# Kernel tuning notes

Hardware: AMD Instinct MI355X
Metric: run time of the kernel (lower is better)

## Reference

```python
import jax, jax.numpy as jnp
import numpy as np

NPOINT = 2048  # S after transition-down (init npoint)
NSAMPLE = 16   # K neighbors (init nsample)
EPS = 1e-5     # BatchNorm eps


def _conv1d(w, b, x):  # w [O,I], x [B,I,N] -> [B,O,N]
    y = jnp.einsum('oi,bin->bon', w, x)
    return y if b is None else y + b[None, :, None]


def _conv2d(w, b, x):  # w [O,I], x [B,I,S,K] -> [B,O,S,K]
    y = jnp.einsum('oi,bisk->bosk', w, x)
    return y if b is None else y + b[None, :, None, None]


def _gather(x, idx):  # x [B,C,N], idx [B,S] -> [B,C,S]
    return jax.vmap(lambda xb, ib: xb[:, ib])(x, idx)


def _group(x, idx):  # x [B,C,N], idx [B,S,K] -> [B,C,S,K]
    return jax.vmap(lambda xb, ib: xb[:, ib])(x, idx)


def _fps(xyz_bnc, S):  # farthest point sampling, start at index 0 (deterministic)
    B, N, _ = xyz_bnc.shape
    def body(carry, _):
        dist, far = carry
        centroid = jnp.take_along_axis(xyz_bnc, far[:, None, None], axis=1)  # [B,1,3]
        d = jnp.sum((xyz_bnc - centroid) ** 2, axis=-1)  # [B,N]
        dist = jnp.minimum(dist, d)
        nxt = jnp.argmax(dist, axis=-1).astype(jnp.int32)
        return (dist, nxt), far
    init = (jnp.full((B, N), 1e10, xyz_bnc.dtype), jnp.zeros((B,), jnp.int32))
    _, idxs = jax.lax.scan(body, init, None, length=S)
    return jnp.transpose(idxs)  # [B,S]


def _knn(k, query, pts):  # query [B,S,3], pts [B,N,3] -> idx [B,S,k]
    d2 = (jnp.sum(query ** 2, -1)[..., None] + jnp.sum(pts ** 2, -1)[:, None, :]
          - 2.0 * jnp.einsum('bsc,bnc->bsn', query, pts))
    _, idx = jax.lax.top_k(-d2, k)
    return idx


def _bn(x, gamma, beta):  # training-mode batchnorm over (B, spatial) per channel
    axes = (0,) + tuple(range(2, x.ndim))
    m = jnp.mean(x, axes, keepdims=True)
    v = jnp.var(x, axes, keepdims=True)
    shp = (1, -1) + (1,) * (x.ndim - 2)
    return gamma.reshape(shp) * (x - m) / jnp.sqrt(v + EPS) + beta.reshape(shp)


def _forward(xyz, points, td_w, td_b, td_gamma, td_beta,
             blk_before_w, blk_before_b, blk_qkv_w,
             blk_pos_w1, blk_pos_b1, blk_pos_w2, blk_pos_b2,
             blk_attn_w1, blk_attn_b1, blk_attn_w2, blk_attn_b2,
             blk_after_w, blk_after_b):
    S, K = NPOINT, NSAMPLE
    xyz_t = jnp.transpose(xyz, (0, 2, 1))  # [B,N,3]
    # ---- PointTransformerTransitionDown ----
    fps_idx = _fps(xyz_t, S)                       # [B,S]
    new_xyz = _gather(xyz, fps_idx)                # [B,3,S]
    new_xyz_t = jnp.transpose(new_xyz, (0, 2, 1))  # [B,S,3]
    gidx = _knn(K, new_xyz_t, xyz_t)               # [B,S,K]
    grouped_xyz = _group(xyz, gidx) - new_xyz[:, :, :, None]   # [B,3,S,K]
    grouped = jnp.concatenate([_group(points, gidx), grouped_xyz], axis=1)  # [B,D+3,S,K]
    h = jax.nn.relu(_bn(_conv2d(td_w, td_b, grouped), td_gamma, td_beta))
    pts = jnp.max(h, axis=-1)  # [B,out,S]
    # ---- PointTransformerResBlocks ----
    sgidx = _knn(K, new_xyz_t, new_xyz_t)          # self-KNN [B,S,K]
    gxyz = new_xyz[:, :, :, None] - _group(new_xyz, sgidx)  # [B,3,S,K]
    num_attn = blk_before_w.shape[0]
    for i in range(num_attn):
        rel = _conv2d(blk_pos_w2[i], blk_pos_b2[i],
                      jax.nn.relu(_conv2d(blk_pos_w1[i], blk_pos_b1[i], gxyz)))  # [B,mid,S,K]
        p = _conv1d(blk_before_w[i], blk_before_b[i], pts)   # [B,mid,S]
        qkv = _conv1d(blk_qkv_w[i], None, p)                 # [B,3*mid,S]
        q, k_, v = jnp.split(qkv, 3, axis=1)
        qk_rel = q[:, :, :, None] - _group(k_, sgidx)        # [B,mid,S,K]
        v = _group(v, sgidx) + rel
        sim = _conv2d(blk_attn_w2[i], blk_attn_b2[i],
                      jax.nn.relu(_conv2d(blk_attn_w1[i], blk_attn_b1[i], qk_rel + rel)))
        attn = jax.nn.softmax(sim, axis=-1)                  # softmax over neighbors
        agg = jnp.sum(attn * v, axis=-1)                     # [B,mid,S]
        pts = pts + _conv1d(blk_after_w[i], blk_after_b[i], agg)
    return new_xyz, pts


def setup_inputs() -> dict:
    key = jax.random.key(0)
    ks = jax.random.split(key, 20)
    B, N, Din, Dout, mid, A = 4, 8192, 64, 128, 32, 2
    r = lambda k, s, sc: sc * jax.random.normal(k, s, dtype=jnp.float32)
    return {
        'xyz': r(ks[0], (B, 3, N), 1.0),
        'points': r(ks[1], (B, Din, N), 1.0),
        'td_w': r(ks[2], (Dout, Din + 3), 0.1), 'td_b': r(ks[3], (Dout,), 0.02),
        'td_gamma': jnp.ones((Dout,), jnp.float32), 'td_beta': jnp.zeros((Dout,), jnp.float32),
        'blk_before_w': r(ks[4], (A, mid, Dout), 0.1), 'blk_before_b': r(ks[5], (A, mid), 0.02),
        'blk_qkv_w': r(ks[6], (A, 3 * mid, mid), 0.1),
        'blk_pos_w1': r(ks[7], (A, 64, 3), 0.1), 'blk_pos_b1': r(ks[8], (A, 64), 0.02),
        'blk_pos_w2': r(ks[9], (A, mid, 64), 0.1), 'blk_pos_b2': r(ks[10], (A, mid), 0.02),
        'blk_attn_w1': r(ks[11], (A, 4 * mid, mid), 0.1), 'blk_attn_b1': r(ks[12], (A, 4 * mid), 0.02),
        'blk_attn_w2': r(ks[13], (A, mid, 4 * mid), 0.1), 'blk_attn_b2': r(ks[14], (A, mid), 0.02),
        'blk_after_w': r(ks[15], (A, Dout, mid), 0.1), 'blk_after_b': r(ks[16], (A, Dout), 0.02),
    }


def reference(xyz, points, td_w, td_b, td_gamma, td_beta,
              blk_before_w, blk_before_b, blk_qkv_w,
              blk_pos_w1, blk_pos_b1, blk_pos_w2, blk_pos_b2,
              blk_attn_w1, blk_attn_b1, blk_attn_w2, blk_attn_b2,
              blk_after_w, blk_after_b):
    return _forward(xyz, points, td_w, td_b, td_gamma, td_beta,
                    blk_before_w, blk_before_b, blk_qkv_w,
                    blk_pos_w1, blk_pos_b1, blk_pos_w2, blk_pos_b2,
                    blk_attn_w1, blk_attn_b1, blk_attn_w2, blk_attn_b2,
                    blk_after_w, blk_after_b)
```

## Files before the change

kernel.cpp:

```cpp
#include <hip/hip_runtime.h>

#define BB 4
#define NN 8192
#define SS 2048
#define KK 16

typedef float v2f __attribute__((ext_vector_type(2)));

#define FTH 512
#define FPT (NN/FTH)
#define TRB 256
#define SPB 124
__global__ __launch_bounds__(FTH, 1) void fps_kernel(
    const float* __restrict__ xyz,
    const float* __restrict__ points,
    float* __restrict__ out_newxyz,
    float* __restrict__ nxt,
    float* __restrict__ ptst,
    int* __restrict__ spin_flag)
{
  #pragma clang fp contract(off)
  const int blk = blockIdx.x;
  const int tid = threadIdx.x;
  __shared__ __align__(16) float4 sxyz[NN];
  __shared__ __align__(16) unsigned long long skey[2][8];
  __shared__ int smi[SS];
  __shared__ float sred[8*6];
  __shared__ float tile[32][33];

  if (blk >= BB) {
    if (blk < BB + TRB) {
      const int x = tid & 31, yy = tid >> 5;
      for (int q = 0; q < 8; ++q) {
        const int tj = (blk - BB)*8 + q;
        const int tn = tj & 255, tc = (tj >> 8) & 1, tb = tj >> 9;
        const int n0 = tn*32, c0 = tc*32;
        __syncthreads();
        tile[yy][x]    = points[(tb*64 + c0+yy)*NN + n0+x];
        tile[yy+16][x] = points[(tb*64 + c0+yy+16)*NN + n0+x];
        __syncthreads();
        ptst[(tb*NN + n0+yy)*64 + c0+x]    = tile[x][yy];
        ptst[(tb*NN + n0+yy+16)*64 + c0+x] = tile[x][yy+16];
      }
      return;
    }
    if (tid >= 64) return;
    const int s0 = atomicAdd(spin_flag, 0);
    float a0 = 1.0f + tid, a1 = 2.0f, a2 = 3.0f, a3 = 4.0f;
    for (int outer = 0; outer < 50000; ++outer) {
      #pragma unroll
      for (int u = 0; u < 256; ++u) {
        a0 = fmaf(a0, 1.0000001f, 1e-7f);
        a1 = fmaf(a1, 0.9999999f, 2e-7f);
        a2 = fmaf(a2, 1.0000002f, 3e-7f);
        a3 = fmaf(a3, 0.9999998f, 4e-7f);
      }
      if (atomicAdd(spin_flag, 0) - s0 >= BB) break;
    }
    asm volatile("" :: "v"(a0), "v"(a1), "v"(a2), "v"(a3));
    return;
  }

  const int b = blk;
  const int wave = tid >> 6;
  const int lane = tid & 63;
  const float* xb = xyz + b*3*NN;

  float tx[FPT], ty[FPT], tz[FPT];
  #pragma unroll
  for (int j = 0; j < FPT; ++j) {
    int i = tid + j*FTH;
    tx[j] = xb[i]; ty[j] = xb[NN+i]; tz[j] = xb[2*NN+i];
  }
  float mnx = tx[0], mxx = tx[0], mny = ty[0], mxy = ty[0], mnz = tz[0], mxz = tz[0];
  #pragma unroll
  for (int j = 1; j < FPT; ++j) {
    mnx = fminf(mnx, tx[j]); mxx = fmaxf(mxx, tx[j]);
    mny = fminf(mny, ty[j]); mxy = fmaxf(mxy, ty[j]);
    mnz = fminf(mnz, tz[j]); mxz = fmaxf(mxz, tz[j]);
  }
  #define WRED(var, OP) { \
    float s_; \
    s_ = __int_as_float(__builtin_amdgcn_update_dpp(0, __float_as_int(var), 0x111, 0xf, 0xf, true)); var = OP(var, s_); \
    s_ = __int_as_float(__builtin_amdgcn_update_dpp(0, __float_as_int(var), 0x112, 0xf, 0xf, true)); var = OP(var, s_); \
    s_ = __int_as_float(__builtin_amdgcn_update_dpp(0, __float_as_int(var), 0x114, 0xf, 0xf, true)); var = OP(var, s_); \
    s_ = __int_as_float(__builtin_amdgcn_update_dpp(0, __float_as_int(var), 0x118, 0xf, 0xf, true)); var = OP(var, s_); \
    s_ = __int_as_float(__builtin_amdgcn_update_dpp(0, __float_as_int(var), 0x142, 0xf, 0xf, true)); var = OP(var, s_); \
    s_ = __int_as_float(__builtin_amdgcn_update_dpp(0, __float_as_int(var), 0x143, 0xf, 0xf, true)); var = OP(var, s_); }
  WRED(mnx, fminf) WRED(mxx, fmaxf) WRED(mny, fminf) WRED(mxy, fmaxf) WRED(mnz, fminf) WRED(mxz, fmaxf)
  #undef WRED
  if (lane == 63) {
    sred[wave*6+0] = mnx; sred[wave*6+1] = mxx; sred[wave*6+2] = mny;
    sred[wave*6+3] = mxy; sred[wave*6+4] = mnz; sred[wave*6+5] = mxz;
  }
  smi[tid] = 0;
  __syncthreads();
  #pragma unroll
  for (int w = 0; w < 8; ++w) {
    mnx = fminf(mnx, sred[w*6+0]); mxx = fmaxf(mxx, sred[w*6+1]);
    mny = fminf(mny, sred[w*6+2]); mxy = fmaxf(mxy, sred[w*6+3]);
    mnz = fminf(mnz, sred[w*6+4]); mxz = fmaxf(mxz, sred[w*6+5]);
  }
  const float scx = 8.0f / (mxx - mnx + 1e-12f);
  const float scy = 8.0f / (mxy - mny + 1e-12f);
  const float scz = 8.0f / (mxz - mnz + 1e-12f);
  int cells[FPT];
  #pragma unroll
  for (int j = 0; j < FPT; ++j) {
    int qx = min(7, (int)((tx[j] - mnx) * scx));
    int qy = min(7, (int)((ty[j] - mny) * scy));
    int qz = min(7, (int)((tz[j] - mnz) * scz));
    int m = (qx&1) | ((qy&1)<<1) | ((qz&1)<<2)
          | ((qx&2)<<2) | ((qy&2)<<3) | ((qz&2)<<4)
          | ((qx&4)<<4) | ((qy&4)<<5) | ((qz&4)<<6);
    cells[j] = m;
    atomicAdd(&smi[m], 1);
  }
  __syncthreads();
  for (int d = 1; d < 512; d <<= 1) {
    int v = smi[tid];
    int a = (tid >= d) ? smi[tid - d] : 0;
    __syncthreads();
    smi[tid] = v + a;
    __syncthreads();
  }
  {
    int excl = (tid == 0) ? 0 : smi[tid - 1];
    smi[512 + tid] = excl;
  }
  __syncthreads();
  #pragma unroll
  for (int j = 0; j < FPT; ++j) {
    int pos = atomicAdd(&smi[512 + cells[j]], 1);
    sxyz[pos] = make_float4(tx[j], ty[j], tz[j], 0.0f);
  }
  __syncthreads();
  v2f px[FPT/2], py[FPT/2], pz[FPT/2], dist[FPT/2];
  float bx0, bx1, by0, by1, bz0, bz1;
  {
    float4 c0 = sxyz[tid*FPT];
    bx0 = bx1 = c0.x; by0 = by1 = c0.y; bz0 = bz1 = c0.z;
    #pragma unroll
    for (int e = 0; e < FPT; ++e) {
      float4 cc = sxyz[tid*FPT + e];
      ((float*)px)[e] = cc.x; ((float*)py)[e] = cc.y; ((float*)pz)[e] = cc.z;
      ((float*)dist)[e] = 1e10f;
      bx0 = fminf(bx0, cc.x); bx1 = fmaxf(bx1, cc.x);
      by0 = fminf(by0, cc.y); by1 = fmaxf(by1, cc.y);
      bz0 = fminf(bz0, cc.z); bz1 = fmaxf(bz1, cc.z);
    }
  }
  float dmax = 1e10f;
  int   beste = 0;
  float cx = xb[0], cy = xb[NN], cz = xb[2*NN];
  __syncthreads();
  for (int it = 1; it < SS; ++it) {
    const int buf = it & 1;
    float gx = fmaxf(fmaxf(bx0 - cx, cx - bx1), 0.0f);
    float gy = fmaxf(fmaxf(by0 - cy, cy - by1), 0.0f);
    float gz = fmaxf(fmaxf(bz0 - cz, cz - bz1), 0.0f);
    float lb = gx*gx + gy*gy; lb = lb + gz*gz;
    if (lb * 0.99999f < dmax) {
      v2f cx2 = {cx, cx}, cy2 = {cy, cy}, cz2 = {cz, cz};
      v2f vmax = {-1.0f, -1.0f};
      #pragma unroll
      for (int j = 0; j < FPT/2; ++j) {
        v2f dx = px[j] - cx2, dy = py[j] - cy2, dz = pz[j] - cz2;
        v2f d = dx*dx + dy*dy;
        d = d + dz*dz;
        v2f nd = __builtin_elementwise_min(dist[j], d);
        dist[j] = nd;
        vmax = __builtin_elementwise_max(vmax, nd);
      }
      float mloc = fmaxf(vmax.x, vmax.y);
      int ce[FPT/2];
      #pragma unroll
      for (int j = 0; j < FPT/2; ++j) {
        int c = 0x7FFFFFFF;
        if (dist[j].y == mloc) c = 2*j + 1;
        if (dist[j].x == mloc) c = 2*j;
        ce[j] = c;
      }
      #pragma unroll
      for (int st = FPT/4; st >= 1; st >>= 1) {
        #pragma unroll
        for (int j = 0; j < st; ++j) ce[j] = ce[j] < ce[j+st] ? ce[j] : ce[j+st];
      }
      dmax = mloc;
      beste = ce[0];
    }
    unsigned khi = __float_as_uint(dmax);
    unsigned klo = ~(unsigned)((tid << 4) + beste);
    #define FPS_RED(ctrl) { \
      unsigned nlo = (unsigned)__builtin_amdgcn_update_dpp(0, (int)klo, ctrl, 0xf, 0xf, true); \
      unsigned nhi = (unsigned)__builtin_amdgcn_update_dpp(0, (int)khi, ctrl, 0xf, 0xf, true); \
      unsigned long long nk = ((unsigned long long)nhi << 32) | nlo; \
      unsigned long long ck = ((unsigned long long)khi << 32) | klo; \
      if (nk > ck) { khi = nhi; klo = nlo; } }
    FPS_RED(0x111)
    FPS_RED(0x112)
    FPS_RED(0x114)
    FPS_RED(0x118)
    FPS_RED(0x142)
    FPS_RED(0x143)
    #undef FPS_RED
    if (lane == 63) skey[buf][wave] = ((unsigned long long)khi << 32) | klo;
    __syncthreads();
    const ulonglong2* kp = (const ulonglong2*)&skey[buf][0];
    ulonglong2 k01 = kp[0], k23 = kp[1], k45 = kp[2], k67 = kp[3];
    unsigned long long m0 = k01.x > k01.y ? k01.x : k01.y;
    unsigned long long m1 = k23.x > k23.y ? k23.x : k23.y;
    unsigned long long m2 = k45.x > k45.y ? k45.x : k45.y;
    unsigned long long m3 = k67.x > k67.y ? k67.x : k67.y;
    unsigned long long ma = m0 > m1 ? m0 : m1;
    unsigned long long mb = m2 > m3 ? m2 : m3;
    unsigned long long mk = ma > mb ? ma : mb;
    int mi = (int)(~(unsigned)mk);
    float4 c = sxyz[mi];
    if (tid == 0) smi[it] = mi;
    cx = c.x; cy = c.y; cz = c.z;
  }
  __syncthreads();
  for (int it = tid; it < SS; it += FTH) {
    float x, y, z;
    if (it == 0) { x = xb[0]; y = xb[NN]; z = xb[2*NN]; }
    else { float4 c = sxyz[smi[it]]; x = c.x; y = c.y; z = c.z; }
    out_newxyz[(b*3+0)*SS + it] = x;
    out_newxyz[(b*3+1)*SS + it] = y;
    out_newxyz[(b*3+2)*SS + it] = z;
    nxt[(b*SS+it)*3+0] = x; nxt[(b*SS+it)*3+1] = y; nxt[(b*SS+it)*3+2] = z;
  }
  if (tid == 0) atomicAdd(spin_flag, 1);
}

#define TILE 2048
#define KTH 512
__global__ __launch_bounds__(KTH) void knn_kernel(
    const float* __restrict__ query_t,
    const float* __restrict__ cand1,
    const float* __restrict__ cand2,
    int* __restrict__ out1,
    int* __restrict__ out2)
{
  #pragma clang fp contract(off)
  __shared__ float4 sc[TILE];
  __shared__ float  smd[8*64*17];
  __shared__ int    smj[8*64*17];
  const int blocksPerB = SS/64;
  const int half = blockIdx.x >> 7;
  const int blk = blockIdx.x & 127;
  const float* cand = half ? cand2 : cand1;
  const int Nc = half ? SS : NN;
  int* outidx = half ? out2 : out1;
  const int b = blk / blocksPerB;
  const int q0 = (blk % blocksPerB)*64;
  const int wave = threadIdx.x >> 6, lane = threadIdx.x & 63;
  const int s = q0 + lane;
  const float qx = query_t[(b*SS+s)*3+0];
  const float qy = query_t[(b*SS+s)*3+1];
  const float qz = query_t[(b*SS+s)*3+2];
  float sq = qx*qx + qy*qy; sq = sq + qz*qz;
  float d16[16]; int i16[16];
  #pragma unroll
  for (int j = 0; j < 16; ++j) { d16[j] = 1e30f; i16[j] = 0x7FFFFFFF; }
  const float* cb = cand + b*3*Nc;
  const int QL = TILE/8;
  for (int base = 0; base < Nc; base += TILE) {
    __syncthreads();
    for (int j = threadIdx.x; j < TILE; j += KTH) {
      float x = cb[base+j], y = cb[Nc+base+j], z = cb[2*Nc+base+j];
      float pp = x*x + y*y; pp = pp + z*z;
      sc[j] = make_float4(x, y, z, pp);
    }
    __syncthreads();
    const int lo = wave*QL, hi = lo + QL;
    for (int j = lo; j < hi; ++j) {
      float4 c = sc[j];
      float qp = qx*c.x + qy*c.y; qp = qp + qz*c.z;
      float d2 = (sq + c.w) - 2.0f*qp;
      if (d2 < d16[15]) {
        d16[15] = d2; i16[15] = base + j;
        #pragma unroll
        for (int t = 15; t > 0; --t) {
          if (d16[t] < d16[t-1]) {
            float td = d16[t]; d16[t] = d16[t-1]; d16[t-1] = td;
            int   ti = i16[t]; i16[t] = i16[t-1]; i16[t-1] = ti;
          }
        }
      }
    }
  }
  const int off = (wave*64 + lane)*17;
  #pragma unroll
  for (int j = 0; j < 16; ++j) { smd[off+j] = d16[j]; smj[off+j] = i16[j]; }
  __syncthreads();
  if (wave == 0) {
    int p[8] = {0,0,0,0,0,0,0,0};
    for (int o = 0; o < 16; ++o) {
      float bd = 3e38f; int bi = 0x7FFFFFFF, bw = 0;
      #pragma unroll
      for (int w = 0; w < 8; ++w) {
        float d = smd[(w*64+lane)*17 + p[w]];
        int   i = smj[(w*64+lane)*17 + p[w]];
        if (d < bd || (d == bd && i < bi)) { bd = d; bi = i; bw = w; }
      }
      p[bw]++;
      outidx[(b*SS+s)*KK + o] = bi;
    }
  }
}

__global__ __launch_bounds__(128) void td_kernel(
    const float* __restrict__ ptst,
    const float* __restrict__ xyz,
    const float* __restrict__ newxyz,
    const int* __restrict__ gidx,
    const float* __restrict__ td_w,
    const float* __restrict__ td_b,
    float* __restrict__ ymax,
    float* __restrict__ psum,
    float* __restrict__ psq)
{
  const int bs = blockIdx.x;
  const int b = bs >> 11, s = bs & (SS-1);
  const int t = threadIdx.x;
  __shared__ int gi[KK];
  __shared__ float g[67*17];
  if (t < KK) gi[t] = gidx[bs*KK + t];
  __syncthreads();
  #pragma unroll
  for (int base = 0; base < 1024; base += 128) {
    int idx = base + t;
    int i = idx & 63, k = idx >> 6;
    g[i*17 + k] = ptst[(b*NN + gi[k])*64 + i];
  }
  if (t < 48) {
    int c = t >> 4, k = t & 15;
    g[(64+c)*17 + k] = xyz[(b*3+c)*NN + gi[k]] - newxyz[(b*3+c)*SS + s];
  }
  __syncthreads();
  float acc[KK];
  #pragma unroll
  for (int k = 0; k < KK; ++k) acc[k] = 0.0f;
  const float* wrow = td_w + t*67;
  for (int i = 0; i < 67; ++i) {
    float w = wrow[i];
    #pragma unroll
    for (int k = 0; k < KK; ++k) acc[k] = fmaf(w, g[i*17 + k], acc[k]);
  }
  float bias = td_b[t];
  float mx = -1e30f, s1 = 0.f, s2 = 0.f;
  #pragma unroll
  for (int k = 0; k < KK; ++k) {
    float y = acc[k] + bias;
    mx = fmaxf(mx, y);
    s1 += y;
    s2 = fmaf(y, y, s2);
  }
  ymax[bs*128 + t] = mx;
  psum[bs*128 + t] = s1;
  psq [bs*128 + t] = s2;
}

__global__ __launch_bounds__(256) void bn_partial(
    const float* __restrict__ psum, const float* __restrict__ psq,
    float* __restrict__ part1, float* __restrict__ part2)
{
  const int blk = blockIdx.x, t = threadIdx.x;
  const int c = t & 127, half = t >> 7;
  const float* ps = psum + (blk*64 + half*32)*128;
  const float* pq = psq  + (blk*64 + half*32)*128;
  float s1 = 0.f, s2 = 0.f;
  for (int r = 0; r < 32; ++r) { s1 += ps[r*128 + c]; s2 += pq[r*128 + c]; }
  __shared__ float sh1[256], sh2[256];
  sh1[t] = s1; sh2[t] = s2;
  __syncthreads();
  if (t < 128) {
    part1[blk*128 + t] = sh1[t] + sh1[t+128];
    part2[blk*128 + t] = sh2[t] + sh2[t+128];
  }
}

__global__ __launch_bounds__(128) void bn_final(
    const float* __restrict__ part1, const float* __restrict__ part2,
    const float* __restrict__ gamma, const float* __restrict__ beta,
    float* __restrict__ scale, float* __restrict__ bias)
{
  const int o = threadIdx.x;
  float s1 = 0.f, s2 = 0.f;
  for (int j = 0; j < 128; ++j) { s1 += part1[j*128+o]; s2 += part2[j*128+o]; }
  const float n = (float)(BB*SS*KK);
  float mean = s1/n;
  float var  = s2/n - mean*mean;
  float sc = gamma[o] / sqrtf(var + 1e-5f);
  scale[o] = sc;
  bias[o]  = beta[o] - mean*sc;
}

__global__ __launch_bounds__(128) void r1_first(
    const float* __restrict__ ymax,
    const float* __restrict__ scale, const float* __restrict__ bias,
    const float* __restrict__ bw, const float* __restrict__ bb,
    const float* __restrict__ qw,
    float* __restrict__ pts,
    float* __restrict__ qkv)
{
  const int bs = blockIdx.x;
  const int t = threadIdx.x;
  __shared__ float pcol[128];
  __shared__ float p[32];
  float v = fmaxf(fmaf(ymax[bs*128 + t], scale[t], bias[t]), 0.0f);
  pts[bs*128 + t] = v;
  pcol[t] = v;
  __syncthreads();
  if (t < 32) {
    float acc = 0.f;
    const float* w = bw + t*128;
    for (int j = 0; j < 128; ++j) acc = fmaf(w[j], pcol[j], acc);
    p[t] = acc + bb[t];
  }
  __syncthreads();
  if (t < 96) {
    float acc = 0.f;
    const float* w = qw + t*32;
    #pragma unroll
    for (int j = 0; j < 32; ++j) acc = fmaf(w[j], p[j], acc);
    qkv[bs*96 + t] = acc;
  }
}

__global__ __launch_bounds__(128) void r1_kernel(
    const float* __restrict__ pts,
    const float* __restrict__ bw, const float* __restrict__ bb,
    const float* __restrict__ qw,
    float* __restrict__ qkv)
{
  const int bs = blockIdx.x;
  const int t = threadIdx.x;
  __shared__ float pcol[128];
  __shared__ float p[32];
  pcol[t] = pts[bs*128 + t];
  __syncthreads();
  if (t < 32) {
    float acc = 0.f;
    const float* w = bw + t*128;
    for (int j = 0; j < 128; ++j) acc = fmaf(w[j], pcol[j], acc);
    p[t] = acc + bb[t];
  }
  __syncthreads();
  if (t < 96) {
    float acc = 0.f;
    const float* w = qw + t*32;
    #pragma unroll
    for (int j = 0; j < 32; ++j) acc = fmaf(w[j], p[j], acc);
    qkv[bs*96 + t] = acc;
  }
}

__global__ __launch_bounds__(128) void r2_kernel(
    const float* __restrict__ qkv,
    const float* __restrict__ newxyz,
    const int* __restrict__ sgidx,
    const float* __restrict__ pw1, const float* __restrict__ pb1,
    const float* __restrict__ pw2, const float* __restrict__ pb2,
    const float* __restrict__ aw1, const float* __restrict__ ab1,
    const float* __restrict__ aw2, const float* __restrict__ ab2,
    const float* __restrict__ fw,  const float* __restrict__ fb,
    float* __restrict__ pts)
{
  const int bs = blockIdx.x;
  const int b = bs >> 11, s = bs & (SS-1);
  const int t = threadIdx.x;
  __shared__ int sgi[KK];
  __shared__ float qv[32];
  __shared__ float kn[32*17], vn[32*17];
  __shared__ float gx[3*KK];
  __shared__ float h1[64*KK];
  __shared__ float x2[32*KK];
  __shared__ float a1[128*17];
  __shared__ float simb[32*KK];
  __shared__ float agg[32];
  if (t < KK) sgi[t] = sgidx[bs*KK + t];
  __syncthreads();
  if (t < 32) qv[t] = qkv[bs*96 + t];
  for (int idx = t; idx < 32*KK; idx += 128) {
    int k = idx >> 5, c = idx & 31;
    int base = (b*SS + sgi[k])*96;
    kn[c*17+k] = qkv[base + 32 + c];
    vn[c*17+k] = qkv[base + 64 + c];
  }
  if (t < 3*KK) {
    int c = t >> 4, k = t & 15;
    gx[t] = newxyz[(b*3+c)*SS + s] - newxyz[(b*3+c)*SS + sgi[k]];
  }
  __syncthreads();
  for (int idx = t; idx < 64*KK; idx += 128) {
    int c = idx >> 4, k = idx & 15;
    float acc = 0.f;
    #pragma unroll
    for (int j = 0; j < 3; ++j) acc = fmaf(pw1[c*3+j], gx[j*KK+k], acc);
    h1[idx] = fmaxf(acc + pb1[c], 0.0f);
  }
  __syncthreads();
  for (int idx = t; idx < 32*KK; idx += 128) {
    int c = idx >> 4, k = idx & 15;
    float acc = 0.f;
    const float* w = pw2 + c*64;
    for (int j = 0; j < 64; ++j) acc = fmaf(w[j], h1[j*KK+k], acc);
    float r = acc + pb2[c];
    x2[idx] = (qv[c] - kn[c*17+k]) + r;
    vn[c*17+k] = vn[c*17+k] + r;
  }
  __syncthreads();
  {
    float acc[KK];
    #pragma unroll
    for (int k = 0; k < KK; ++k) acc[k] = 0.f;
    const float* w = aw1 + t*32;
    for (int j = 0; j < 32; ++j) {
      float wv = w[j];
      #pragma unroll
      for (int k = 0; k < KK; ++k) acc[k] = fmaf(wv, x2[j*KK+k], acc[k]);
    }
    float bv = ab1[t];
    #pragma unroll
    for (int k = 0; k < KK; ++k) a1[t*17+k] = fmaxf(acc[k] + bv, 0.0f);
  }
  __syncthreads();
  for (int idx = t; idx < 32*KK; idx += 128) {
    int c = idx >> 4, k = idx & 15;
    float acc = 0.f;
    const float* w = aw2 + c*128;
    for (int j = 0; j < 128; ++j) acc = fmaf(w[j], a1[j*17+k], acc);
    simb[idx] = acc + ab2[c];
  }
  __syncthreads();
  if (t < 32) {
    float m = -1e30f;
    #pragma unroll
    for (int k = 0; k < KK; ++k) m = fmaxf(m, simb[t*KK+k]);
    float sum = 0.f;
    float e[KK];
    #pragma unroll
    for (int k = 0; k < KK; ++k) { e[k] = __expf(simb[t*KK+k] - m); sum += e[k]; }
    float inv = 1.0f / sum;
    float a = 0.f;
    #pragma unroll
    for (int k = 0; k < KK; ++k) a = fmaf(e[k]*inv, vn[t*17+k], a);
    agg[t] = a;
  }
  __syncthreads();
  {
    float acc = 0.f;
    const float* w = fw + t*32;
    #pragma unroll
    for (int j = 0; j < 32; ++j) acc = fmaf(w[j], agg[j], acc);
    pts[bs*128 + t] += acc + fb[t];
  }
}

__global__ __launch_bounds__(256) void transpose_out(
    const float* __restrict__ pts, float* __restrict__ out)
{
  __shared__ float tile[32][33];
  const int b = blockIdx.z;
  const int s0 = blockIdx.x*32, c0 = blockIdx.y*32;
  const int x = threadIdx.x, y = threadIdx.y;
  #pragma unroll
  for (int i = y; i < 32; i += 8)
    tile[i][x] = pts[(b*SS + s0+i)*128 + c0+x];
  __syncthreads();
  #pragma unroll
  for (int i = y; i < 32; i += 8)
    out[(b*128 + c0+i)*SS + s0 + x] = tile[x][i];
}

extern "C" void kernel_launch(void* const* d_in, const int* in_sizes, int n_in,
                              void* d_out, int out_size, void* d_ws, size_t ws_size,
                              hipStream_t stream) {
  const float* xyz      = (const float*)d_in[0];
  const float* points   = (const float*)d_in[1];
  const float* td_w     = (const float*)d_in[2];
  const float* td_b     = (const float*)d_in[3];
  const float* td_gamma = (const float*)d_in[4];
  const float* td_beta  = (const float*)d_in[5];
  const float* bw  = (const float*)d_in[6];
  const float* bb  = (const float*)d_in[7];
  const float* qw  = (const float*)d_in[8];
  const float* pw1 = (const float*)d_in[9];
  const float* pb1 = (const float*)d_in[10];
  const float* pw2 = (const float*)d_in[11];
  const float* pb2 = (const float*)d_in[12];
  const float* aw1 = (const float*)d_in[13];
  const float* ab1 = (const float*)d_in[14];
  const float* aw2 = (const float*)d_in[15];
  const float* ab2 = (const float*)d_in[16];
  const float* fw  = (const float*)d_in[17];
  const float* fb  = (const float*)d_in[18];
  float* out = (float*)d_out;
  float* out_newxyz = out;
  float* out_pts    = out + BB*3*SS;

  char* w = (char*)d_ws;
  float* nxt    = (float*)w; w += BB*SS*3*sizeof(float);
  int*   gidx   = (int*)w;   w += BB*SS*KK*sizeof(int);
  int*   sgidx  = (int*)w;   w += BB*SS*KK*sizeof(int);
  float* ymax   = (float*)w; w += BB*128*SS*sizeof(float);
  float* psum   = (float*)w; w += 128*BB*SS*sizeof(float);
  float* psq    = (float*)w; w += 128*BB*SS*sizeof(float);
  float* part1  = (float*)w; w += 128*128*sizeof(float);
  float* part2  = (float*)w; w += 128*128*sizeof(float);
  float* bnscale= (float*)w; w += 256*sizeof(float);
  float* bnbias = (float*)w; w += 256*sizeof(float);
  float* pts    = (float*)w; w += BB*128*SS*sizeof(float);
  float* qkv    = (float*)w; w += BB*96*SS*sizeof(float);
  float* ptst   = (float*)w; w += BB*NN*64*sizeof(float);
  int*   spinflag = (int*)w; w += 256;

  fps_kernel<<<BB + TRB + SPB, FTH, 0, stream>>>(xyz, points, out_newxyz, nxt, ptst, spinflag);
  knn_kernel<<<2*BB*(SS/64), KTH, 0, stream>>>(nxt, xyz, out_newxyz, gidx, sgidx);
  td_kernel<<<BB*SS, 128, 0, stream>>>(ptst, xyz, out_newxyz, gidx, td_w, td_b, ymax, psum, psq);
  bn_partial<<<128, 256, 0, stream>>>(psum, psq, part1, part2);
  bn_final<<<1, 128, 0, stream>>>(part1, part2, td_gamma, td_beta, bnscale, bnbias);
  r1_first<<<BB*SS, 128, 0, stream>>>(ymax, bnscale, bnbias, bw, bb, qw, pts, qkv);
  r2_kernel<<<BB*SS, 128, 0, stream>>>(qkv, out_newxyz, sgidx,
      pw1, pb1, pw2, pb2, aw1, ab1, aw2, ab2, fw, fb, pts);
  r1_kernel<<<BB*SS, 128, 0, stream>>>(pts, bw + 32*128, bb + 32, qw + 96*32, qkv);
  r2_kernel<<<BB*SS, 128, 0, stream>>>(qkv, out_newxyz, sgidx,
      pw1 + 64*3, pb1 + 64, pw2 + 32*64, pb2 + 32,
      aw1 + 128*32, ab1 + 128, aw2 + 32*128, ab2 + 32,
      fw + 128*32, fb + 128, pts);
  dim3 tg(SS/32, 128/32, BB), tb(32, 8);
  transpose_out<<<tg, tb, 0, stream>>>(pts, out_pts);
}
```

Before: 2.408 ms.

## Fuse FPS, KNN and transition-down into one persistent kernel with flag sync

Combines the FPS, KNN and td kernels into a single persistent 256-block launch. Four blocks run FPS while the others transpose points. All blocks then pull KNN and td work units from atomic counters, waiting on global flag barriers between phases. This removes the spin-heater blocks and two launch boundaries so idle CUs can start KNN as soon as FPS finishes. In exchange it relies on all 256 blocks being co-resident, and the td unit now uses 4 groups of 128 threads per block instead of one small block per point.

Result: slower. 3.079 ms (+27.9%).

```diff
diff --git a/kernel.cpp b/kernel.cpp
--- a/kernel.cpp
+++ b/kernel.cpp
@@ -4,251 +4,50 @@
 #define NN 8192
 #define SS 2048
 #define KK 16
+#define TILE 2048
 
 typedef float v2f __attribute__((ext_vector_type(2)));
 
 #define FTH 512
 #define FPT (NN/FTH)
-#define TRB 256
-#define SPB 124
-__global__ __launch_bounds__(FTH, 1) void fps_kernel(
-    const float* __restrict__ xyz,
-    const float* __restrict__ points,
-    float* __restrict__ out_newxyz,
-    float* __restrict__ nxt,
-    float* __restrict__ ptst,
-    int* __restrict__ spin_flag)
-{
+#define NWORK 252
+
+struct SMemF {
+  float4 sxyz[NN];
+  unsigned long long skey[2][8];
+  int smi[SS];
+  float sred[8*6];
+};
+struct SMemW {
+  float tile[32][33];
+  float4 sc[TILE];
+  float  smd[8*64*17];
+  int    smj[8*64*17];
+};
+struct SMemT {
+  int   gi[4][KK];
+  float g[4][67*17];
+};
+union SMemU { SMemF f; SMemW w; SMemT t; };
+
+__device__ __forceinline__ void wait_count(int* f, unsigned base, unsigned target) {
+  if (threadIdx.x == 0) {
+    for (int it = 0; it < 200000; ++it) {
+      if ((unsigned)atomicAdd(f, 0) - base >= target) break;
+      __builtin_amdgcn_s_sleep(64);
+    }
+  }
+  __syncthreads();
+  __threadfence();
+}
+
+__device__ void knn_unit(SMemW& sw, int u, const float* __restrict__ query_t,
+                         const float* __restrict__ cand1, const float* __restrict__ cand2,
+                         int* __restrict__ out1, int* __restrict__ out2) {
   #pragma clang fp contract(off)
-  const int blk = blockIdx.x;
-  const int tid = threadIdx.x;
-  __shared__ __align__(16) float4 sxyz[NN];
-  __shared__ __align__(16) unsigned long long skey[2][8];
-  __shared__ int smi[SS];
-  __shared__ float sred[8*6];
-  __shared__ float tile[32][33];
-
-  if (blk >= BB) {
-    if (blk < BB + TRB) {
-      const int x = tid & 31, yy = tid >> 5;
-      for (int q = 0; q < 8; ++q) {
-        const int tj = (blk - BB)*8 + q;
-        const int tn = tj & 255, tc = (tj >> 8) & 1, tb = tj >> 9;
-        const int n0 = tn*32, c0 = tc*32;
-        __syncthreads();
-        tile[yy][x]    = points[(tb*64 + c0+yy)*NN + n0+x];
-        tile[yy+16][x] = points[(tb*64 + c0+yy+16)*NN + n0+x];
-        __syncthreads();
-        ptst[(tb*NN + n0+yy)*64 + c0+x]    = tile[x][yy];
-        ptst[(tb*NN + n0+yy+16)*64 + c0+x] = tile[x][yy+16];
-      }
-      return;
-    }
-    if (tid >= 64) return;
-    const int s0 = atomicAdd(spin_flag, 0);
-    float a0 = 1.0f + tid, a1 = 2.0f, a2 = 3.0f, a3 = 4.0f;
-    for (int outer = 0; outer < 50000; ++outer) {
-      #pragma unroll
-      for (int u = 0; u < 256; ++u) {
-        a0 = fmaf(a0, 1.0000001f, 1e-7f);
-        a1 = fmaf(a1, 0.9999999f, 2e-7f);
-        a2 = fmaf(a2, 1.0000002f, 3e-7f);
-        a3 = fmaf(a3, 0.9999998f, 4e-7f);
-      }
-      if (atomicAdd(spin_flag, 0) - s0 >= BB) break;
-    }
-    asm volatile("" :: "v"(a0), "v"(a1), "v"(a2), "v"(a3));
-    return;
-  }
-
-  const int b = blk;
-  const int wave = tid >> 6;
-  const int lane = tid & 63;
-  const float* xb = xyz + b*3*NN;
-
-  float tx[FPT], ty[FPT], tz[FPT];
-  #pragma unroll
-  for (int j = 0; j < FPT; ++j) {
-    int i = tid + j*FTH;
-    tx[j] = xb[i]; ty[j] = xb[NN+i]; tz[j] = xb[2*NN+i];
-  }
-  float mnx = tx[0], mxx = tx[0], mny = ty[0], mxy = ty[0], mnz = tz[0], mxz = tz[0];
-  #pragma unroll
-  for (int j = 1; j < FPT; ++j) {
-    mnx = fminf(mnx, tx[j]); mxx = fmaxf(mxx, tx[j]);
-    mny = fminf(mny, ty[j]); mxy = fmaxf(mxy, ty[j]);
-    mnz = fminf(mnz, tz[j]); mxz = fmaxf(mxz, tz[j]);
-  }
-  #define WRED(var, OP) { \
-    float s_; \
-    s_ = __int_as_float(__builtin_amdgcn_update_dpp(0, __float_as_int(var), 0x111, 0xf, 0xf, true)); var = OP(var, s_); \
-    s_ = __int_as_float(__builtin_amdgcn_update_dpp(0, __float_as_int(var), 0x112, 0xf, 0xf, true)); var = OP(var, s_); \
-    s_ = __int_as_float(__builtin_amdgcn_update_dpp(0, __float_as_int(var), 0x114, 0xf, 0xf, true)); var = OP(var, s_); \
-    s_ = __int_as_float(__builtin_amdgcn_update_dpp(0, __float_as_int(var), 0x118, 0xf, 0xf, true)); var = OP(var, s_); \
-    s_ = __int_as_float(__builtin_amdgcn_update_dpp(0, __float_as_int(var), 0x142, 0xf, 0xf, true)); var = OP(var, s_); \
-    s_ = __int_as_float(__builtin_amdgcn_update_dpp(0, __float_as_int(var), 0x143, 0xf, 0xf, true)); var = OP(var, s_); }
-  WRED(mnx, fminf) WRED(mxx, fmaxf) WRED(mny, fminf) WRED(mxy, fmaxf) WRED(mnz, fminf) WRED(mxz, fmaxf)
-  #undef WRED
-  if (lane == 63) {
-    sred[wave*6+0] = mnx; sred[wave*6+1] = mxx; sred[wave*6+2] = mny;
-    sred[wave*6+3] = mxy; sred[wave*6+4] = mnz; sred[wave*6+5] = mxz;
-  }
-  smi[tid] = 0;
-  __syncthreads();
-  #pragma unroll
-  for (int w = 0; w < 8; ++w) {
-    mnx = fminf(mnx, sred[w*6+0]); mxx = fmaxf(mxx, sred[w*6+1]);
-    mny = fminf(mny, sred[w*6+2]); mxy = fmaxf(mxy, sred[w*6+3]);
-    mnz = fminf(mnz, sred[w*6+4]); mxz = fmaxf(mxz, sred[w*6+5]);
-  }
-  const float scx = 8.0f / (mxx - mnx + 1e-12f);
-  const float scy = 8.0f / (mxy - mny + 1e-12f);
-  const float scz = 8.0f / (mxz - mnz + 1e-12f);
-  int cells[FPT];
-  #pragma unroll
-  for (int j = 0; j < FPT; ++j) {
-    int qx = min(7, (int)((tx[j] - mnx) * scx));
-    int qy = min(7, (int)((ty[j] - mny) * scy));
-    int qz = min(7, (int)((tz[j] - mnz) * scz));
-    int m = (qx&1) | ((qy&1)<<1) | ((qz&1)<<2)
-          | ((qx&2)<<2) | ((qy&2)<<3) | ((qz&2)<<4)
-          | ((qx&4)<<4) | ((qy&4)<<5) | ((qz&4)<<6);
-    cells[j] = m;
-    atomicAdd(&smi[m], 1);
-  }
-  __syncthreads();
-  for (int d = 1; d < 512; d <<= 1) {
-    int v = smi[tid];
-    int a = (tid >= d) ? smi[tid - d] : 0;
-    __syncthreads();
-    smi[tid] = v + a;
-    __syncthreads();
-  }
-  {
-    int excl = (tid == 0) ? 0 : smi[tid - 1];
-    smi[512 + tid] = excl;
-  }
-  __syncthreads();
-  #pragma unroll
-  for (int j = 0; j < FPT; ++j) {
-    int pos = atomicAdd(&smi[512 + cells[j]], 1);
-    sxyz[pos] = make_float4(tx[j], ty[j], tz[j], 0.0f);
-  }
-  __syncthreads();
-  v2f px[FPT/2], py[FPT/2], pz[FPT/2], dist[FPT/2];
-  float bx0, bx1, by0, by1, bz0, bz1;
-  {
-    float4 c0 = sxyz[tid*FPT];
-    bx0 = bx1 = c0.x; by0 = by1 = c0.y; bz0 = bz1 = c0.z;
-    #pragma unroll
-    for (int e = 0; e < FPT; ++e) {
-      float4 cc = sxyz[tid*FPT + e];
-      ((float*)px)[e] = cc.x; ((float*)py)[e] = cc.y; ((float*)pz)[e] = cc.z;
-      ((float*)dist)[e] = 1e10f;
-      bx0 = fminf(bx0, cc.x); bx1 = fmaxf(bx1, cc.x);
-      by0 = fminf(by0, cc.y); by1 = fmaxf(by1, cc.y);
-      bz0 = fminf(bz0, cc.z); bz1 = fmaxf(bz1, cc.z);
-    }
-  }
-  float dmax = 1e10f;
-  int   beste = 0;
-  float cx = xb[0], cy = xb[NN], cz = xb[2*NN];
-  __syncthreads();
-  for (int it = 1; it < SS; ++it) {
-    const int buf = it & 1;
-    float gx = fmaxf(fmaxf(bx0 - cx, cx - bx1), 0.0f);
-    float gy = fmaxf(fmaxf(by0 - cy, cy - by1), 0.0f);
-    float gz = fmaxf(fmaxf(bz0 - cz, cz - bz1), 0.0f);
-    float lb = gx*gx + gy*gy; lb = lb + gz*gz;
-    if (lb * 0.99999f < dmax) {
-      v2f cx2 = {cx, cx}, cy2 = {cy, cy}, cz2 = {cz, cz};
-      v2f vmax = {-1.0f, -1.0f};
-      #pragma unroll
-      for (int j = 0; j < FPT/2; ++j) {
-        v2f dx = px[j] - cx2, dy = py[j] - cy2, dz = pz[j] - cz2;
-        v2f d = dx*dx + dy*dy;
-        d = d + dz*dz;
-        v2f nd = __builtin_elementwise_min(dist[j], d);
-        dist[j] = nd;
-        vmax = __builtin_elementwise_max(vmax, nd);
-      }
-      float mloc = fmaxf(vmax.x, vmax.y);
-      int ce[FPT/2];
-      #pragma unroll
-      for (int j = 0; j < FPT/2; ++j) {
-        int c = 0x7FFFFFFF;
-        if (dist[j].y == mloc) c = 2*j + 1;
-        if (dist[j].x == mloc) c = 2*j;
-        ce[j] = c;
-      }
-      #pragma unroll
-      for (int st = FPT/4; st >= 1; st >>= 1) {
-        #pragma unroll
-        for (int j = 0; j < st; ++j) ce[j] = ce[j] < ce[j+st] ? ce[j] : ce[j+st];
-      }
-      dmax = mloc;
-      beste = ce[0];
-    }
-    unsigned khi = __float_as_uint(dmax);
-    unsigned klo = ~(unsigned)((tid << 4) + beste);
-    #define FPS_RED(ctrl) { \
-      unsigned nlo = (unsigned)__builtin_amdgcn_update_dpp(0, (int)klo, ctrl, 0xf, 0xf, true); \
-      unsigned nhi = (unsigned)__builtin_amdgcn_update_dpp(0, (int)khi, ctrl, 0xf, 0xf, true); \
-      unsigned long long nk = ((unsigned long long)nhi << 32) | nlo; \
-      unsigned long long ck = ((unsigned long long)khi << 32) | klo; \
-      if (nk > ck) { khi = nhi; klo = nlo; } }
-    FPS_RED(0x111)
-    FPS_RED(0x112)
-    FPS_RED(0x114)
-    FPS_RED(0x118)
-    FPS_RED(0x142)
-    FPS_RED(0x143)
-    #undef FPS_RED
-    if (lane == 63) skey[buf][wave] = ((unsigned long long)khi << 32) | klo;
-    __syncthreads();
-    const ulonglong2* kp = (const ulonglong2*)&skey[buf][0];
-    ulonglong2 k01 = kp[0], k23 = kp[1], k45 = kp[2], k67 = kp[3];
-    unsigned long long m0 = k01.x > k01.y ? k01.x : k01.y;
-    unsigned long long m1 = k23.x > k23.y ? k23.x : k23.y;
-    unsigned long long m2 = k45.x > k45.y ? k45.x : k45.y;
-    unsigned long long m3 = k67.x > k67.y ? k67.x : k67.y;
-    unsigned long long ma = m0 > m1 ? m0 : m1;
-    unsigned long long mb = m2 > m3 ? m2 : m3;
-    unsigned long long mk = ma > mb ? ma : mb;
-    int mi = (int)(~(unsigned)mk);
-    float4 c = sxyz[mi];
-    if (tid == 0) smi[it] = mi;
-    cx = c.x; cy = c.y; cz = c.z;
-  }
-  __syncthreads();
-  for (int it = tid; it < SS; it += FTH) {
-    float x, y, z;
-    if (it == 0) { x = xb[0]; y = xb[NN]; z = xb[2*NN]; }
-    else { float4 c = sxyz[smi[it]]; x = c.x; y = c.y; z = c.z; }
-    out_newxyz[(b*3+0)*SS + it] = x;
-    out_newxyz[(b*3+1)*SS + it] = y;
-    out_newxyz[(b*3+2)*SS + it] = z;
-    nxt[(b*SS+it)*3+0] = x; nxt[(b*SS+it)*3+1] = y; nxt[(b*SS+it)*3+2] = z;
-  }
-  if (tid == 0) atomicAdd(spin_flag, 1);
-}
-
-#define TILE 2048
-#define KTH 512
-__global__ __launch_bounds__(KTH) void knn_kernel(
-    const float* __restrict__ query_t,
-    const float* __restrict__ cand1,
-    const float* __restrict__ cand2,
-    int* __restrict__ out1,
-    int* __restrict__ out2)
-{
-  #pragma clang fp contract(off)
-  __shared__ float4 sc[TILE];
-  __shared__ float  smd[8*64*17];
-  __shared__ int    smj[8*64*17];
   const int blocksPerB = SS/64;
-  const int half = blockIdx.x >> 7;
-  const int blk = blockIdx.x & 127;
+  const int half = u >> 7;
+  const int blk = u & 127;
   const float* cand = half ? cand2 : cand1;
   const int Nc = half ? SS : NN;
   int* outidx = half ? out2 : out1;
@@ -267,15 +66,15 @@
   const int QL = TILE/8;
   for (int base = 0; base < Nc; base += TILE) {
     __syncthreads();
-    for (int j = threadIdx.x; j < TILE; j += KTH) {
+    for (int j = threadIdx.x; j < TILE; j += FTH) {
       float x = cb[base+j], y = cb[Nc+base+j], z = cb[2*Nc+base+j];
       float pp = x*x + y*y; pp = pp + z*z;
-      sc[j] = make_float4(x, y, z, pp);
+      sw.sc[j] = make_float4(x, y, z, pp);
     }
     __syncthreads();
     const int lo = wave*QL, hi = lo + QL;
     for (int j = lo; j < hi; ++j) {
-      float4 c = sc[j];
+      float4 c = sw.sc[j];
       float qp = qx*c.x + qy*c.y; qp = qp + qz*c.z;
       float d2 = (sq + c.w) - 2.0f*qp;
       if (d2 < d16[15]) {
@@ -292,7 +91,7 @@
   }
   const int off = (wave*64 + lane)*17;
   #pragma unroll
-  for (int j = 0; j < 16; ++j) { smd[off+j] = d16[j]; smj[off+j] = i16[j]; }
+  for (int j = 0; j < 16; ++j) { sw.smd[off+j] = d16[j]; sw.smj[off+j] = i16[j]; }
   __syncthreads();
   if (wave == 0) {
     int p[8] = {0,0,0,0,0,0,0,0};
@@ -300,8 +99,8 @@
       float bd = 3e38f; int bi = 0x7FFFFFFF, bw = 0;
       #pragma unroll
       for (int w = 0; w < 8; ++w) {
-        float d = smd[(w*64+lane)*17 + p[w]];
-        int   i = smj[(w*64+lane)*17 + p[w]];
+        float d = sw.smd[(w*64+lane)*17 + p[w]];
+        int   i = sw.smj[(w*64+lane)*17 + p[w]];
         if (d < bd || (d == bd && i < bi)) { bd = d; bi = i; bw = w; }
       }
       p[bw]++;
@@ -310,56 +109,294 @@
   }
 }
 
-__global__ __launch_bounds__(128) void td_kernel(
-    const float* __restrict__ ptst,
+__device__ void td_unit(SMemT& st, int v, const float* __restrict__ ptst,
+                        const float* __restrict__ xyz, const float* __restrict__ newxyz,
+                        const int* __restrict__ gidx, const float* __restrict__ td_w,
+                        const float* __restrict__ td_b,
+                        float* __restrict__ ymax, float* __restrict__ psum, float* __restrict__ psq) {
+  const int grp = threadIdx.x >> 7;
+  const int t = threadIdx.x & 127;
+  int*   gi = st.gi[grp];
+  float* g  = st.g[grp];
+  for (int r = 0; r < 16; ++r) {
+    const int bs = v*64 + r*4 + grp;
+    const int b = bs >> 11, s = bs & (SS-1);
+    __syncthreads();
+    if (t < KK) gi[t] = gidx[bs*KK + t];
+    __syncthreads();
+    #pragma unroll
+    for (int base = 0; base < 1024; base += 128) {
+      int idx = base + t;
+      int i = idx & 63, k = idx >> 6;
+      g[i*17 + k] = ptst[(b*NN + gi[k])*64 + i];
+    }
+    if (t < 48) {
+      int c = t >> 4, k = t & 15;
+      g[(64+c)*17 + k] = xyz[(b*3+c)*NN + gi[k]] - newxyz[(b*3+c)*SS + s];
+    }
+    __syncthreads();
+    float acc[KK];
+    #pragma unroll
+    for (int k = 0; k < KK; ++k) acc[k] = 0.0f;
+    const float* wrow = td_w + t*67;
+    for (int i = 0; i < 67; ++i) {
+      float w = wrow[i];
+      #pragma unroll
+      for (int k = 0; k < KK; ++k) acc[k] = fmaf(w, g[i*17 + k], acc[k]);
+    }
+    float bias = td_b[t];
+    float mx = -1e30f, s1 = 0.f, s2 = 0.f;
+    #pragma unroll
+    for (int k = 0; k < KK; ++k) {
+      float y = acc[k] + bias;
+      mx = fmaxf(mx, y);
+      s1 += y;
+      s2 = fmaf(y, y, s2);
+    }
+    ymax[bs*128 + t] = mx;
+    psum[bs*128 + t] = s1;
+    psq [bs*128 + t] = s2;
+  }
+}
+
+__global__ __launch_bounds__(FTH, 1) void mega_kernel(
     const float* __restrict__ xyz,
-    const float* __restrict__ newxyz,
-    const int* __restrict__ gidx,
-    const float* __restrict__ td_w,
-    const float* __restrict__ td_b,
-    float* __restrict__ ymax,
-    float* __restrict__ psum,
-    float* __restrict__ psq)
+    const float* __restrict__ points,
+    const float* __restrict__ td_w, const float* __restrict__ td_b,
+    float* __restrict__ out_newxyz,
+    float* __restrict__ nxt,
+    float* __restrict__ ptst,
+    int* __restrict__ gidx, int* __restrict__ sgidx,
+    float* __restrict__ ymax, float* __restrict__ psum, float* __restrict__ psq,
+    int* flags)
 {
-  const int bs = blockIdx.x;
-  const int b = bs >> 11, s = bs & (SS-1);
-  const int t = threadIdx.x;
-  __shared__ int gi[KK];
-  __shared__ float g[67*17];
-  if (t < KK) gi[t] = gidx[bs*KK + t];
-  __syncthreads();
-  #pragma unroll
-  for (int base = 0; base < 1024; base += 128) {
-    int idx = base + t;
-    int i = idx & 63, k = idx >> 6;
-    g[i*17 + k] = ptst[(b*NN + gi[k])*64 + i];
-  }
-  if (t < 48) {
-    int c = t >> 4, k = t & 15;
-    g[(64+c)*17 + k] = xyz[(b*3+c)*NN + gi[k]] - newxyz[(b*3+c)*SS + s];
-  }
-  __syncthreads();
-  float acc[KK];
-  #pragma unroll
-  for (int k = 0; k < KK; ++k) acc[k] = 0.0f;
-  const float* wrow = td_w + t*67;
-  for (int i = 0; i < 67; ++i) {
-    float w = wrow[i];
-    #pragma unroll
-    for (int k = 0; k < KK; ++k) acc[k] = fmaf(w, g[i*17 + k], acc[k]);
-  }
-  float bias = td_b[t];
-  float mx = -1e30f, s1 = 0.f, s2 = 0.f;
-  #pragma unroll
-  for (int k = 0; k < KK; ++k) {
-    float y = acc[k] + bias;
-    mx = fmaxf(mx, y);
-    s1 += y;
-    s2 = fmaf(y, y, s2);
-  }
-  ymax[bs*128 + t] = mx;
-  psum[bs*128 + t] = s1;
-  psq [bs*128 + t] = s2;
+  #pragma clang fp contract(off)
+  const int blk = blockIdx.x;
+  const int tid = threadIdx.x;
+  __shared__ SMemU sm;
+  __shared__ int s_unit;
+
+  unsigned b0 = 0, b1 = 0, b2 = 0, b3 = 0, b4 = 0;
+  if (tid == 0) {
+    b0 = (unsigned)atomicAdd(&flags[0], 0);
+    b1 = (unsigned)atomicAdd(&flags[1], 0);
+    b2 = (unsigned)atomicAdd(&flags[2], 0);
+    b3 = (unsigned)atomicAdd(&flags[3], 0);
+    b4 = (unsigned)atomicAdd(&flags[4], 0);
+  }
+
+  if (blk < BB) {
+    const int b = blk;
+    const int wave = tid >> 6;
+    const int lane = tid & 63;
+    const float* xb = xyz + b*3*NN;
+    float tx[FPT], ty[FPT], tz[FPT];
+    #pragma unroll
+    for (int j = 0; j < FPT; ++j) {
+      int i = tid + j*FTH;
+      tx[j] = xb[i]; ty[j] = xb[NN+i]; tz[j] = xb[2*NN+i];
+    }
+    float mnx = tx[0], mxx = tx[0], mny = ty[0], mxy = ty[0], mnz = tz[0], mxz = tz[0];
+    #pragma unroll
+    for (int j = 1; j < FPT; ++j) {
+      mnx = fminf(mnx, tx[j]); mxx = fmaxf(mxx, tx[j]);
+      mny = fminf(mny, ty[j]); mxy = fmaxf(mxy, ty[j]);
+      mnz = fminf(mnz, tz[j]); mxz = fmaxf(mxz, tz[j]);
+    }
+    #define WRED(var, OP) { \
+      float s_; \
+      s_ = __int_as_float(__builtin_amdgcn_update_dpp(0, __float_as_int(var), 0x111, 0xf, 0xf, true)); var = OP(var, s_); \
+      s_ = __int_as_float(__builtin_amdgcn_update_dpp(0, __float_as_int(var), 0x112, 0xf, 0xf, true)); var = OP(var, s_); \
+      s_ = __int_as_float(__builtin_amdgcn_update_dpp(0, __float_as_int(var), 0x114, 0xf, 0xf, true)); var = OP(var, s_); \
+      s_ = __int_as_float(__builtin_amdgcn_update_dpp(0, __float_as_int(var), 0x118, 0xf, 0xf, true)); var = OP(var, s_); \
+      s_ = __int_as_float(__builtin_amdgcn_update_dpp(0, __float_as_int(var), 0x142, 0xf, 0xf, true)); var = OP(var, s_); \
+      s_ = __int_as_float(__builtin_amdgcn_update_dpp(0, __float_as_int(var), 0x143, 0xf, 0xf, true)); var = OP(var, s_); }
+    WRED(mnx, fminf) WRED(mxx, fmaxf) WRED(mny, fminf) WRED(mxy, fmaxf) WRED(mnz, fminf) WRED(mxz, fmaxf)
+    #undef WRED
+    if (lane == 63) {
+      sm.f.sred[wave*6+0] = mnx; sm.f.sred[wave*6+1] = mxx; sm.f.sred[wave*6+2] = mny;
+      sm.f.sred[wave*6+3] = mxy; sm.f.sred[wave*6+4] = mnz; sm.f.sred[wave*6+5] = mxz;
+    }
+    sm.f.smi[tid] = 0;
+    __syncthreads();
+    #pragma unroll
+    for (int w = 0; w < 8; ++w) {
+      mnx = fminf(mnx, sm.f.sred[w*6+0]); mxx = fmaxf(mxx, sm.f.sred[w*6+1]);
+      mny = fminf(mny, sm.f.sred[w*6+2]); mxy = fmaxf(mxy, sm.f.sred[w*6+3]);
+      mnz = fminf(mnz, sm.f.sred[w*6+4]); mxz = fmaxf(mxz, sm.f.sred[w*6+5]);
+    }
+    const float scx = 8.0f / (mxx - mnx + 1e-12f);
+    const float scy = 8.0f / (mxy - mny + 1e-12f);
+    const float scz = 8.0f / (mxz - mnz + 1e-12f);
+    int cells[FPT];
+    #pragma unroll
+    for (int j = 0; j < FPT; ++j) {
+      int qx = min(7, (int)((tx[j] - mnx) * scx));
+      int qy = min(7, (int)((ty[j] - mny) * scy));
+      int qz = min(7, (int)((tz[j] - mnz) * scz));
+      int m = (qx&1) | ((qy&1)<<1) | ((qz&1)<<2)
+            | ((qx&2)<<2) | ((qy&2)<<3) | ((qz&2)<<4)
+            | ((qx&4)<<4) | ((qy&4)<<5) | ((qz&4)<<6);
+      cells[j] = m;
+      atomicAdd(&sm.f.smi[m], 1);
+    }
+    __syncthreads();
+    for (int d = 1; d < 512; d <<= 1) {
+      int v = sm.f.smi[tid];
+      int a = (tid >= d) ? sm.f.smi[tid - d] : 0;
+      __syncthreads();
+      sm.f.smi[tid] = v + a;
+      __syncthreads();
+    }
+    {
+      int excl = (tid == 0) ? 0 : sm.f.smi[tid - 1];
+      sm.f.smi[512 + tid] = excl;
+    }
+    __syncthreads();
+    #pragma unroll
+    for (int j = 0; j < FPT; ++j) {
+      int pos = atomicAdd(&sm.f.smi[512 + cells[j]], 1);
+      sm.f.sxyz[pos] = make_float4(tx[j], ty[j], tz[j], 0.0f);
+    }
+    __syncthreads();
+    v2f px[FPT/2], py[FPT/2], pz[FPT/2], dist[FPT/2];
+    float bx0, bx1, by0, by1, bz0, bz1;
+    {
+      float4 c0 = sm.f.sxyz[tid*FPT];
+      bx0 = bx1 = c0.x; by0 = by1 = c0.y; bz0 = bz1 = c0.z;
+      #pragma unroll
+      for (int e = 0; e < FPT; ++e) {
+        float4 cc = sm.f.sxyz[tid*FPT + e];
+        ((float*)px)[e] = cc.x; ((float*)py)[e] = cc.y; ((float*)pz)[e] = cc.z;
+        ((float*)dist)[e] = 1e10f;
+        bx0 = fminf(bx0, cc.x); bx1 = fmaxf(bx1, cc.x);
+        by0 = fminf(by0, cc.y); by1 = fmaxf(by1, cc.y);
+        bz0 = fminf(bz0, cc.z); bz1 = fmaxf(bz1, cc.z);
+      }
+    }
+    float dmax = 1e10f;
+    int   beste = 0;
+    float cx = xb[0], cy = xb[NN], cz = xb[2*NN];
+    __syncthreads();
+    for (int it = 1; it < SS; ++it) {
+      const int buf = it & 1;
+      float gx = fmaxf(fmaxf(bx0 - cx, cx - bx1), 0.0f);
+      float gy = fmaxf(fmaxf(by0 - cy, cy - by1), 0.0f);
+      float gz = fmaxf(fmaxf(bz0 - cz, cz - bz1), 0.0f);
+      float lb = gx*gx + gy*gy; lb = lb + gz*gz;
+      if (lb * 0.99999f < dmax) {
+        v2f cx2 = {cx, cx}, cy2 = {cy, cy}, cz2 = {cz, cz};
+        v2f vmax = {-1.0f, -1.0f};
+        #pragma unroll
+        for (int j = 0; j < FPT/2; ++j) {
+          v2f dx = px[j] - cx2, dy = py[j] - cy2, dz = pz[j] - cz2;
+          v2f d = dx*dx + dy*dy;
+          d = d + dz*dz;
+          v2f nd = __builtin_elementwise_min(dist[j], d);
+          dist[j] = nd;
+          vmax = __builtin_elementwise_max(vmax, nd);
+        }
+        float mloc = fmaxf(vmax.x, vmax.y);
+        int ce[FPT/2];
+        #pragma unroll
+        for (int j = 0; j < FPT/2; ++j) {
+          int c = 0x7FFFFFFF;
+          if (dist[j].y == mloc) c = 2*j + 1;
+          if (dist[j].x == mloc) c = 2*j;
+          ce[j] = c;
+        }
+        #pragma unroll
+        for (int st = FPT/4; st >= 1; st >>= 1) {
+          #pragma unroll
+          for (int j = 0; j < st; ++j) ce[j] = ce[j] < ce[j+st] ? ce[j] : ce[j+st];
+        }
+        dmax = mloc;
+        beste = ce[0];
+      }
+      unsigned khi = __float_as_uint(dmax);
+      unsigned klo = ~(unsigned)((tid << 4) + beste);
+      #define FPS_RED(ctrl) { \
+        unsigned nlo = (unsigned)__builtin_amdgcn_update_dpp(0, (int)klo, ctrl, 0xf, 0xf, true); \
+        unsigned nhi = (unsigned)__builtin_amdgcn_update_dpp(0, (int)khi, ctrl, 0xf, 0xf, true); \
+        unsigned long long nk = ((unsigned long long)nhi << 32) | nlo; \
+        unsigned long long ck = ((unsigned long long)khi << 32) | klo; \
+        if (nk > ck) { khi = nhi; klo = nlo; } }
+      FPS_RED(0x111)
+      FPS_RED(0x112)
+      FPS_RED(0x114)
+      FPS_RED(0x118)
+      FPS_RED(0x142)
+      FPS_RED(0x143)
+      #undef FPS_RED
+      if (lane == 63) sm.f.skey[buf][wave] = ((unsigned long long)khi << 32) | klo;
+      __syncthreads();
+      const ulonglong2* kp = (const ulonglong2*)&sm.f.skey[buf][0];
+      ulonglong2 k01 = kp[0], k23 = kp[1], k45 = kp[2], k67 = kp[3];
+      unsigned long long m0 = k01.x > k01.y ? k01.x : k01.y;
+      unsigned long long m1 = k23.x > k23.y ? k23.x : k23.y;
+      unsigned long long m2 = k45.x > k45.y ? k45.x : k45.y;
+      unsigned long long m3 = k67.x > k67.y ? k67.x : k67.y;
+      unsigned long long ma = m0 > m1 ? m0 : m1;
+      unsigned long long mb = m2 > m3 ? m2 : m3;
+      unsigned long long mk = ma > mb ? ma : mb;
+      int mi = (int)(~(unsigned)mk);
+      float4 c = sm.f.sxyz[mi];
+      if (tid == 0) sm.f.smi[it] = mi;
+      cx = c.x; cy = c.y; cz = c.z;
+    }
+    __syncthreads();
+    for (int it = tid; it < SS; it += FTH) {
+      float x, y, z;
+      if (it == 0) { x = xb[0]; y = xb[NN]; z = xb[2*NN]; }
+      else { float4 c = sm.f.sxyz[sm.f.smi[it]]; x = c.x; y = c.y; z = c.z; }
+      out_newxyz[(b*3+0)*SS + it] = x;
+      out_newxyz[(b*3+1)*SS + it] = y;
+      out_newxyz[(b*3+2)*SS + it] = z;
+      nxt[(b*SS+it)*3+0] = x; nxt[(b*SS+it)*3+1] = y; nxt[(b*SS+it)*3+2] = z;
+    }
+    __syncthreads();
+    __threadfence();
+    if (tid == 0) atomicAdd(&flags[0], 1);
+  } else {
+    const int widx = blk - BB;
+    const int x = tid & 31, yy = tid >> 5;
+    for (int tj = widx; tj < 2048; tj += NWORK) {
+      const int tn = tj & 255, tc = (tj >> 8) & 1, tb = tj >> 9;
+      const int n0 = tn*32, c0 = tc*32;
+      __syncthreads();
+      sm.w.tile[yy][x]    = points[(tb*64 + c0+yy)*NN + n0+x];
+      sm.w.tile[yy+16][x] = points[(tb*64 + c0+yy+16)*NN + n0+x];
+      __syncthreads();
+      ptst[(tb*NN + n0+yy)*64 + c0+x]    = sm.w.tile[x][yy];
+      ptst[(tb*NN + n0+yy+16)*64 + c0+x] = sm.w.tile[x][yy+16];
+    }
+    __syncthreads();
+    __threadfence();
+    if (tid == 0) atomicAdd(&flags[2], 1);
+  }
+
+  wait_count(&flags[0], b0, BB);
+  for (;;) {
+    __syncthreads();
+    if (tid == 0) s_unit = (int)((unsigned)atomicAdd(&flags[1], 1) - b1);
+    __syncthreads();
+    const int u = s_unit;
+    if (u >= 256) break;
+    knn_unit(sm.w, u, nxt, xyz, out_newxyz, gidx, sgidx);
+  }
+  __syncthreads();
+  __threadfence();
+  if (tid == 0) atomicAdd(&flags[3], 1);
+  wait_count(&flags[3], b3, 256);
+  wait_count(&flags[2], b2, NWORK);
+  for (;;) {
+    __syncthreads();
+    if (tid == 0) s_unit = (int)((unsigned)atomicAdd(&flags[4], 1) - b4);
+    __syncthreads();
+    const int v = s_unit;
+    if (v >= 128) break;
+    td_unit(sm.t, v, ptst, xyz, out_newxyz, gidx, td_w, td_b, ymax, psum, psq);
+  }
 }
 
 __global__ __launch_bounds__(256) void bn_partial(
@@ -615,11 +652,10 @@
   float* pts    = (float*)w; w += BB*128*SS*sizeof(float);
   float* qkv    = (float*)w; w += BB*96*SS*sizeof(float);
   float* ptst   = (float*)w; w += BB*NN*64*sizeof(float);
-  int*   spinflag = (int*)w; w += 256;
-
-  fps_kernel<<<BB + TRB + SPB, FTH, 0, stream>>>(xyz, points, out_newxyz, nxt, ptst, spinflag);
-  knn_kernel<<<2*BB*(SS/64), KTH, 0, stream>>>(nxt, xyz, out_newxyz, gidx, sgidx);
-  td_kernel<<<BB*SS, 128, 0, stream>>>(ptst, xyz, out_newxyz, gidx, td_w, td_b, ymax, psum, psq);
+  int*   flags  = (int*)w;   w += 256;
+
+  mega_kernel<<<256, FTH, 0, stream>>>(xyz, points, td_w, td_b,
+      out_newxyz, nxt, ptst, gidx, sgidx, ymax, psum, psq, flags);
   bn_partial<<<128, 256, 0, stream>>>(psum, psq, part1, part2);
   bn_final<<<1, 128, 0, stream>>>(part1, part2, td_gamma, td_beta, bnscale, bnbias);
   r1_first<<<BB*SS, 128, 0, stream>>>(ymax, bnscale, bnbias, bw, bb, qw, pts, qkv);
```
